# Optimization experiments

Hardware: AMD Instinct MI355X
Metric: run time of the kernel (lower is better)

## Reference

```python
import jax, jax.numpy as jnp
import numpy as np

B, IN, J, K = 1024, 512, 64, 8
CLAMP_MAX = 10.0

def setup_inputs() -> dict:
    key = jax.random.key(0)
    k1, k2 = jax.random.split(key)
    x = jax.random.normal(k1, (B, IN), dtype=jnp.float32)
    T = jax.random.normal(k2, (IN, J, K), dtype=jnp.float32)
    return {"x": x, "T": T}

def reference(x, T):
    # M: [B, J, K]
    M = jnp.einsum('bi,ijk->bjk', x, T)
    # pairwise diff over batch: [B, B, J, K] (matches torch broadcast M1-M2)
    diff = M[None, :, :, :] - M[:, None, :, :]
    sq = jnp.sum(diff * diff, axis=3)          # [B, B, J]
    # safe sqrt (grad 0 at 0, matching torch.norm subgradient on diagonal)
    sq_safe = jnp.where(sq > 0, sq, 1.0)
    norm = jnp.where(sq > 0, jnp.sqrt(sq_safe), 0.0)
    c = jnp.exp(-jnp.minimum(norm, CLAMP_MAX))  # clamp(max=10) then exp(-.)
    feats = jnp.sum(c, axis=1)                  # [B, J]
    return jnp.concatenate([x, feats], axis=1)  # [B, IN + J]
```

## Files before the change

kernel.cpp:

```cpp
#include <hip/hip_runtime.h>

constexpr int NB  = 1024;
constexpr int NIN = 512;
constexpr int NJ  = 64;
constexpr int NK  = 8;
constexpr int NC  = NJ * NK;
constexpr int OUTC = NIN + NJ;
constexpr float EXPN10 = 4.5399929762484854e-05f;
constexpr float FEAT_BASE = 1024.0f * EXPN10;

typedef __bf16 bf16x8 __attribute__((ext_vector_type(8)));
typedef float floatx16 __attribute__((ext_vector_type(16)));

__device__ __forceinline__ unsigned f2bf(float f) {
  unsigned u = __float_as_uint(f);
  u += 0x7FFFu + ((u >> 16) & 1u);
  return u >> 16;
}

__global__ __launch_bounds__(256) void conv_init_kernel(const float* __restrict__ x,
                                                        const float* __restrict__ T,
                                                        uint4* __restrict__ xb,
                                                        ushort* __restrict__ Tt,
                                                        float* __restrict__ out) {
  __shared__ float Ts[64][65];
  const int bid = blockIdx.x;
  const int tid = threadIdx.x;

  if (bid < 256) {
    const int idx = bid * 256 + tid;
    const float4 v0 = ((const float4*)x)[idx * 2];
    const float4 v1 = ((const float4*)x)[idx * 2 + 1];
    uint4 p;
    p.x = f2bf(v0.x) | (f2bf(v0.y) << 16);
    p.y = f2bf(v0.z) | (f2bf(v0.w) << 16);
    p.z = f2bf(v1.x) | (f2bf(v1.y) << 16);
    p.w = f2bf(v1.z) | (f2bf(v1.w) << 16);
    xb[idx] = p;
  } else if (bid < 320) {
    const int t = bid - 256;
    const int i0 = (t & 7) * 64;
    const int c0 = (t >> 3) * 64;

    const int ti4 = (tid >> 4) * 4;
    const int tc  = (tid & 15) * 4;
#pragma unroll
    for (int r = 0; r < 4; ++r) {
      const float4 v = *(const float4*)&T[(i0 + ti4 + r) * NC + c0 + tc];
      Ts[tc + 0][ti4 + r] = v.x;
      Ts[tc + 1][ti4 + r] = v.y;
      Ts[tc + 2][ti4 + r] = v.z;
      Ts[tc + 3][ti4 + r] = v.w;
    }
    __syncthreads();

    const int co = tid >> 2;
    const int io = (tid & 3) * 16;
    unsigned w[8];
#pragma unroll
    for (int q = 0; q < 8; ++q)
      w[q] = f2bf(Ts[co][io + 2 * q]) | (f2bf(Ts[co][io + 2 * q + 1]) << 16);
    uint4* dst = (uint4*)&Tt[(size_t)(c0 + co) * NIN + i0 + io];
    dst[0] = uint4{w[0], w[1], w[2], w[3]};
    dst[1] = uint4{w[4], w[5], w[6], w[7]};
  } else {
    const int idx = (bid - 320) * 256 + tid;
    const int b = idx / OUTC;
    const int c = idx - b * OUTC;
    out[idx] = (c < NIN) ? x[b * NIN + c] : FEAT_BASE;
  }
}

__global__ __launch_bounds__(256) void gemm_kernel(const uint4* __restrict__ xb,
                                                   const uint4* __restrict__ ttb,
                                                   float* __restrict__ Mp,
                                                   uint4* __restrict__ Mb,
                                                   float* __restrict__ na) {
  __shared__ __align__(16) ushort smem_u[2 * 64 * 136];
  ushort* Xs = smem_u;
  ushort* Ts = smem_u + 64 * 136;
  float*  Cs = (float*)smem_u;

  const int tid = threadIdx.x;
  const int b0 = blockIdx.x * 64;
  const int c0 = blockIdx.y * 64;

  const int lane = tid & 63;
  const int w    = tid >> 6;
  const int l31  = lane & 31;
  const int half = lane >> 5;
  const int arow = (w & 1) * 32 + l31;
  const int bcol = (w >> 1) * 32 + l31;

  floatx16 acc = {};

  for (int z = 0; z < 4; ++z) {
#pragma unroll
    for (int t = 0; t < 4; ++t) {
      const int u = t * 256 + tid;
      const int row = u >> 4, seg = u & 15;
      *(uint4*)&Xs[row * 136 + seg * 8] = xb[(b0 + row) * 64 + z * 16 + seg];
      *(uint4*)&Ts[row * 136 + seg * 8] = ttb[(c0 + row) * 64 + z * 16 + seg];
    }
    __syncthreads();

#pragma unroll
    for (int s = 0; s < 8; ++s) {
      const bf16x8 af = *(const bf16x8*)&Xs[arow * 136 + s * 16 + half * 8];
      const bf16x8 bf = *(const bf16x8*)&Ts[bcol * 136 + s * 16 + half * 8];
      acc = __builtin_amdgcn_mfma_f32_32x32x16_bf16(af, bf, acc, 0, 0, 0);
    }
    __syncthreads();
  }

#pragma unroll
  for (int reg = 0; reg < 16; ++reg) {
    const int row = (reg & 3) + 8 * (reg >> 2) + 4 * half;
    Cs[((w & 1) * 32 + row) * 68 + (w >> 1) * 32 + l31] = acc[reg];
  }
  __syncthreads();

#pragma unroll
  for (int pass = 0; pass < 2; ++pass) {
    const int jl = (tid >> 6) + pass * 4;
    const int b  = tid & 63;
    const float4 m0 = *(const float4*)&Cs[b * 68 + jl * 8];
    const float4 m1 = *(const float4*)&Cs[b * 68 + jl * 8 + 4];
    const int j_g = blockIdx.y * 8 + jl;
    const int idx = j_g * NB + b0 + b;
    ((float4*)Mp)[idx * 2]     = m0;
    ((float4*)Mp)[idx * 2 + 1] = m1;
    float s = m0.x * m0.x;
    s = fmaf(m0.y, m0.y, s); s = fmaf(m0.z, m0.z, s); s = fmaf(m0.w, m0.w, s);
    s = fmaf(m1.x, m1.x, s); s = fmaf(m1.y, m1.y, s); s = fmaf(m1.z, m1.z, s);
    s = fmaf(m1.w, m1.w, s);
    na[idx] = s;
    uint4 pk;
    pk.x = f2bf(m0.x) | (f2bf(m0.y) << 16);
    pk.y = f2bf(m0.z) | (f2bf(m0.w) << 16);
    pk.z = f2bf(m1.x) | (f2bf(m1.y) << 16);
    pk.w = f2bf(m1.z) | (f2bf(m1.w) << 16);
    Mb[idx] = pk;
  }
}

__global__ __launch_bounds__(256) void pairwise_kernel(const uint4* __restrict__ Mb,
                                                       const float* __restrict__ na,
                                                       const float* __restrict__ Mp,
                                                       float* __restrict__ out) {
  const int j    = blockIdx.x;
  const int ag   = blockIdx.y;
  const int bh   = blockIdx.z;
  const int tid  = threadIdx.x;
  const int lane = tid & 63;
  const int w    = tid >> 6;
  const int col  = lane & 31;
  const int h    = lane >> 5;
  const int jb   = j * NB;

  __shared__ uint4 Mb_s[513];
  __shared__ float nb_s[512];
  __shared__ float na_s[128];

  const int bbeg = bh * 512;
  Mb_s[tid]       = Mb[jb + bbeg + tid];
  Mb_s[tid + 256] = Mb[jb + bbeg + tid + 256];
  nb_s[tid]       = na[jb + bbeg + tid];
  nb_s[tid + 256] = na[jb + bbeg + tid + 256];
  if (tid == 0) Mb_s[512] = uint4{0u, 0u, 0u, 0u};

  const int a0 = ag * 128 + w * 32;
  if (lane < 32) na_s[w * 32 + lane] = na[jb + a0 + lane];

  uint4 araw = uint4{0u, 0u, 0u, 0u};
  if (lane < 32) araw = Mb[jb + a0 + lane];
  const bf16x8 af = __builtin_bit_cast(bf16x8, araw);

  __syncthreads();

  float c995[16];
#pragma unroll
  for (int reg = 0; reg < 16; ++reg) {
    const int row = (reg & 3) + 8 * (reg >> 2) + 4 * h;
    c995[reg] = 0.995f * na_s[w * 32 + row];
  }

  const floatx16 zero = {};

#pragma unroll 2
  for (int bt = 0; bt < 16; ++bt) {
    const int bidx = bt * 32 + col;
    const uint4 braw = Mb_s[lane < 32 ? bidx : 512];
    const bf16x8 bf = __builtin_bit_cast(bf16x8, braw);
    const floatx16 P = __builtin_amdgcn_mfma_f32_32x32x16_bf16(af, bf, zero, 0, 0, 0);
    const float nb_l = nb_s[bidx];
    const float rhs = 100.0f - 0.995f * nb_l;

    float t = fmaf(-2.0f, P[0], c995[0]);
#pragma unroll
    for (int reg = 1; reg < 16; ++reg)
      t = fminf(t, fmaf(-2.0f, P[reg], c995[reg]));

    if (__any(t < rhs)) {
#pragma unroll
      for (int reg = 0; reg < 16; ++reg) {
        if (fmaf(-2.0f, P[reg], c995[reg]) < rhs) {
          const int row = (reg & 3) + 8 * (reg >> 2) + 4 * h;
          const int a = a0 + row;
          const int b = bbeg + bt * 32 + col;
          float corr;
          if (a == b) {
            corr = 1.0f - EXPN10;
          } else {
            const float4 av0 = ((const float4*)Mp)[(jb + a) * 2];
            const float4 av1 = ((const float4*)Mp)[(jb + a) * 2 + 1];
            const float4 bv0 = ((const float4*)Mp)[(jb + b) * 2];
            const float4 bv1 = ((const float4*)Mp)[(jb + b) * 2 + 1];
            float d = av0.x - bv0.x; float sq = d * d;
            d = av0.y - bv0.y; sq = fmaf(d, d, sq);
            d = av0.z - bv0.z; sq = fmaf(d, d, sq);
            d = av0.w - bv0.w; sq = fmaf(d, d, sq);
            d = av1.x - bv1.x; sq = fmaf(d, d, sq);
            d = av1.y - bv1.y; sq = fmaf(d, d, sq);
            d = av1.z - bv1.z; sq = fmaf(d, d, sq);
            d = av1.w - bv1.w; sq = fmaf(d, d, sq);
            const float nrm = sqrtf(sq);
            corr = (nrm < 10.0f) ? (__expf(-nrm) - EXPN10) : 0.0f;
          }
          if (corr != 0.0f) atomicAdd(&out[a * OUTC + NIN + j], corr);
        }
      }
    }
  }
}

extern "C" void kernel_launch(void* const* d_in, const int* in_sizes, int n_in,
                              void* d_out, int out_size, void* d_ws, size_t ws_size,
                              hipStream_t stream) {
  const float* x = (const float*)d_in[0];
  const float* T = (const float*)d_in[1];
  float* out = (float*)d_out;

  float* Mp  = (float*)d_ws;
  float* na  = Mp + (size_t)NJ * NB * NK;
  uint4* Mb  = (uint4*)(na + (size_t)NJ * NB);
  uint4* xb  = Mb + (size_t)NJ * NB;
  ushort* Tt = (ushort*)(xb + (size_t)NB * NIN / 8);

  conv_init_kernel<<<dim3(2624), 256, 0, stream>>>(x, T, xb, Tt, out);
  gemm_kernel<<<dim3(16, 8), 256, 0, stream>>>(xb, (const uint4*)Tt, Mp, Mb, na);
  pairwise_kernel<<<dim3(NJ, 8, 2), 256, 0, stream>>>(Mb, na, Mp, out);
}
```

Baseline: 73.71 us.

## Fuse GEMM and pairwise kernels with a grid-wide atomic barrier

Merges the GEMM stage, the output initialisation (now float4-vectorised) and the pairwise stage into one persistent launch of 1024 blocks. A global atomic counter barrier, reset by the conversion kernel, separates the two phases. The aim is to remove one kernel launch and its inter-kernel gap and to overlap output init with the GEMM. It relies on all 1024 blocks being co-resident (launch bounds 256,4); otherwise the spin barrier can deadlock, and every block pays the barrier cost.

```diff
diff --git a/kernel.cpp b/kernel.cpp
--- a/kernel.cpp
+++ b/kernel.cpp
@@ -9,6 +9,8 @@
 constexpr float EXPN10 = 4.5399929762484854e-05f;
 constexpr float FEAT_BASE = 1024.0f * EXPN10;
 
+constexpr unsigned GRID2 = 1024;
+
 typedef __bf16 bf16x8 __attribute__((ext_vector_type(8)));
 typedef float floatx16 __attribute__((ext_vector_type(16)));
 
@@ -18,14 +20,16 @@
   return u >> 16;
 }
 
-__global__ __launch_bounds__(256) void conv_init_kernel(const float* __restrict__ x,
-                                                        const float* __restrict__ T,
-                                                        uint4* __restrict__ xb,
-                                                        ushort* __restrict__ Tt,
-                                                        float* __restrict__ out) {
+__global__ __launch_bounds__(256) void conv_kernel(const float* __restrict__ x,
+                                                   const float* __restrict__ T,
+                                                   uint4* __restrict__ xb,
+                                                   ushort* __restrict__ Tt,
+                                                   unsigned* __restrict__ cnt) {
   __shared__ float Ts[64][65];
   const int bid = blockIdx.x;
   const int tid = threadIdx.x;
+
+  if (bid == 0 && tid == 0) *cnt = 0u;
 
   if (bid < 256) {
     const int idx = bid * 256 + tid;
@@ -37,7 +41,7 @@
     p.z = f2bf(v1.x) | (f2bf(v1.y) << 16);
     p.w = f2bf(v1.z) | (f2bf(v1.w) << 16);
     xb[idx] = p;
-  } else if (bid < 320) {
+  } else {
     const int t = bid - 256;
     const int i0 = (t & 7) * 64;
     const int c0 = (t >> 3) * 64;
@@ -63,104 +67,120 @@
     uint4* dst = (uint4*)&Tt[(size_t)(c0 + co) * NIN + i0 + io];
     dst[0] = uint4{w[0], w[1], w[2], w[3]};
     dst[1] = uint4{w[4], w[5], w[6], w[7]};
+  }
+}
+
+__global__ __launch_bounds__(256, 4) void fused_kernel(const uint4* __restrict__ xb,
+                                                       const uint4* __restrict__ ttb,
+                                                       const float* __restrict__ x,
+                                                       float* __restrict__ Mp,
+                                                       uint4* __restrict__ Mb,
+                                                       float* __restrict__ na,
+                                                       float* __restrict__ out,
+                                                       unsigned* __restrict__ cnt) {
+  __shared__ __align__(16) unsigned char smem[2 * 64 * 136 * 2];
+  const int tid = threadIdx.x;
+  const int bid = blockIdx.x;
+
+  if (bid < 128) {
+    ushort* Xs = (ushort*)smem;
+    ushort* Ts = (ushort*)smem + 64 * 136;
+    float*  Cs = (float*)smem;
+
+    const int b0 = (bid & 15) * 64;
+    const int c0 = (bid >> 4) * 64;
+
+    const int lane = tid & 63;
+    const int w    = tid >> 6;
+    const int l31  = lane & 31;
+    const int half = lane >> 5;
+    const int arow = (w & 1) * 32 + l31;
+    const int bcol = (w >> 1) * 32 + l31;
+
+    floatx16 acc = {};
+
+    for (int z = 0; z < 4; ++z) {
+#pragma unroll
+      for (int t = 0; t < 4; ++t) {
+        const int u = t * 256 + tid;
+        const int row = u >> 4, seg = u & 15;
+        *(uint4*)&Xs[row * 136 + seg * 8] = xb[(b0 + row) * 64 + z * 16 + seg];
+        *(uint4*)&Ts[row * 136 + seg * 8] = ttb[(c0 + row) * 64 + z * 16 + seg];
+      }
+      __syncthreads();
+
+#pragma unroll
+      for (int s = 0; s < 8; ++s) {
+        const bf16x8 af = *(const bf16x8*)&Xs[arow * 136 + s * 16 + half * 8];
+        const bf16x8 bf = *(const bf16x8*)&Ts[bcol * 136 + s * 16 + half * 8];
+        acc = __builtin_amdgcn_mfma_f32_32x32x16_bf16(af, bf, acc, 0, 0, 0);
+      }
+      __syncthreads();
+    }
+
+#pragma unroll
+    for (int reg = 0; reg < 16; ++reg) {
+      const int row = (reg & 3) + 8 * (reg >> 2) + 4 * half;
+      Cs[((w & 1) * 32 + row) * 68 + (w >> 1) * 32 + l31] = acc[reg];
+    }
+    __syncthreads();
+
+#pragma unroll
+    for (int pass = 0; pass < 2; ++pass) {
+      const int jl = (tid >> 6) + pass * 4;
+      const int b  = tid & 63;
+      const float4 m0 = *(const float4*)&Cs[b * 68 + jl * 8];
+      const float4 m1 = *(const float4*)&Cs[b * 68 + jl * 8 + 4];
+      const int j_g = (bid >> 4) * 8 + jl;
+      const int idx = j_g * NB + b0 + b;
+      ((float4*)Mp)[idx * 2]     = m0;
+      ((float4*)Mp)[idx * 2 + 1] = m1;
+      float s = m0.x * m0.x;
+      s = fmaf(m0.y, m0.y, s); s = fmaf(m0.z, m0.z, s); s = fmaf(m0.w, m0.w, s);
+      s = fmaf(m1.x, m1.x, s); s = fmaf(m1.y, m1.y, s); s = fmaf(m1.z, m1.z, s);
+      s = fmaf(m1.w, m1.w, s);
+      na[idx] = s;
+      uint4 pk;
+      pk.x = f2bf(m0.x) | (f2bf(m0.y) << 16);
+      pk.y = f2bf(m0.z) | (f2bf(m0.w) << 16);
+      pk.z = f2bf(m1.x) | (f2bf(m1.y) << 16);
+      pk.w = f2bf(m1.z) | (f2bf(m1.w) << 16);
+      Mb[idx] = pk;
+    }
   } else {
-    const int idx = (bid - 320) * 256 + tid;
-    const int b = idx / OUTC;
-    const int c = idx - b * OUTC;
-    out[idx] = (c < NIN) ? x[b * NIN + c] : FEAT_BASE;
-  }
-}
-
-__global__ __launch_bounds__(256) void gemm_kernel(const uint4* __restrict__ xb,
-                                                   const uint4* __restrict__ ttb,
-                                                   float* __restrict__ Mp,
-                                                   uint4* __restrict__ Mb,
-                                                   float* __restrict__ na) {
-  __shared__ __align__(16) ushort smem_u[2 * 64 * 136];
-  ushort* Xs = smem_u;
-  ushort* Ts = smem_u + 64 * 136;
-  float*  Cs = (float*)smem_u;
-
-  const int tid = threadIdx.x;
-  const int b0 = blockIdx.x * 64;
-  const int c0 = blockIdx.y * 64;
-
-  const int lane = tid & 63;
-  const int w    = tid >> 6;
-  const int l31  = lane & 31;
-  const int half = lane >> 5;
-  const int arow = (w & 1) * 32 + l31;
-  const int bcol = (w >> 1) * 32 + l31;
-
-  floatx16 acc = {};
-
-  for (int z = 0; z < 4; ++z) {
-#pragma unroll
-    for (int t = 0; t < 4; ++t) {
-      const int u = t * 256 + tid;
-      const int row = u >> 4, seg = u & 15;
-      *(uint4*)&Xs[row * 136 + seg * 8] = xb[(b0 + row) * 64 + z * 16 + seg];
-      *(uint4*)&Ts[row * 136 + seg * 8] = ttb[(c0 + row) * 64 + z * 16 + seg];
-    }
-    __syncthreads();
-
-#pragma unroll
-    for (int s = 0; s < 8; ++s) {
-      const bf16x8 af = *(const bf16x8*)&Xs[arow * 136 + s * 16 + half * 8];
-      const bf16x8 bf = *(const bf16x8*)&Ts[bcol * 136 + s * 16 + half * 8];
-      acc = __builtin_amdgcn_mfma_f32_32x32x16_bf16(af, bf, acc, 0, 0, 0);
-    }
-    __syncthreads();
-  }
-
-#pragma unroll
-  for (int reg = 0; reg < 16; ++reg) {
-    const int row = (reg & 3) + 8 * (reg >> 2) + 4 * half;
-    Cs[((w & 1) * 32 + row) * 68 + (w >> 1) * 32 + l31] = acc[reg];
-  }
+    const int gi = (bid - 128) * 256 + tid;
+    if (gi < (NB * OUTC) / 4) {
+      const int b = gi / (OUTC / 4);
+      const int r = gi - b * (OUTC / 4);
+      float4 v;
+      if (r < NIN / 4) v = ((const float4*)x)[b * (NIN / 4) + r];
+      else v = float4{FEAT_BASE, FEAT_BASE, FEAT_BASE, FEAT_BASE};
+      ((float4*)out)[gi] = v;
+    }
+  }
+
   __syncthreads();
-
-#pragma unroll
-  for (int pass = 0; pass < 2; ++pass) {
-    const int jl = (tid >> 6) + pass * 4;
-    const int b  = tid & 63;
-    const float4 m0 = *(const float4*)&Cs[b * 68 + jl * 8];
-    const float4 m1 = *(const float4*)&Cs[b * 68 + jl * 8 + 4];
-    const int j_g = blockIdx.y * 8 + jl;
-    const int idx = j_g * NB + b0 + b;
-    ((float4*)Mp)[idx * 2]     = m0;
-    ((float4*)Mp)[idx * 2 + 1] = m1;
-    float s = m0.x * m0.x;
-    s = fmaf(m0.y, m0.y, s); s = fmaf(m0.z, m0.z, s); s = fmaf(m0.w, m0.w, s);
-    s = fmaf(m1.x, m1.x, s); s = fmaf(m1.y, m1.y, s); s = fmaf(m1.z, m1.z, s);
-    s = fmaf(m1.w, m1.w, s);
-    na[idx] = s;
-    uint4 pk;
-    pk.x = f2bf(m0.x) | (f2bf(m0.y) << 16);
-    pk.y = f2bf(m0.z) | (f2bf(m0.w) << 16);
-    pk.z = f2bf(m1.x) | (f2bf(m1.y) << 16);
-    pk.w = f2bf(m1.z) | (f2bf(m1.w) << 16);
-    Mb[idx] = pk;
-  }
-}
-
-__global__ __launch_bounds__(256) void pairwise_kernel(const uint4* __restrict__ Mb,
-                                                       const float* __restrict__ na,
-                                                       const float* __restrict__ Mp,
-                                                       float* __restrict__ out) {
-  const int j    = blockIdx.x;
-  const int ag   = blockIdx.y;
-  const int bh   = blockIdx.z;
-  const int tid  = threadIdx.x;
+  if (tid == 0) {
+    __threadfence();
+    __hip_atomic_fetch_add(cnt, 1u, __ATOMIC_ACQ_REL, __HIP_MEMORY_SCOPE_AGENT);
+    while (__hip_atomic_load(cnt, __ATOMIC_ACQUIRE, __HIP_MEMORY_SCOPE_AGENT) < GRID2)
+      __builtin_amdgcn_s_sleep(2);
+    __threadfence();
+  }
+  __syncthreads();
+
+  const int j    = bid & 63;
+  const int ag   = (bid >> 6) & 7;
+  const int bh   = bid >> 9;
   const int lane = tid & 63;
   const int w    = tid >> 6;
   const int col  = lane & 31;
   const int h    = lane >> 5;
   const int jb   = j * NB;
 
-  __shared__ uint4 Mb_s[513];
-  __shared__ float nb_s[512];
-  __shared__ float na_s[128];
+  uint4* Mb_s = (uint4*)smem;
+  float* nb_s = (float*)(smem + 8208);
+  float* na_s = (float*)(smem + 10256);
 
   const int bbeg = bh * 512;
   Mb_s[tid]       = Mb[jb + bbeg + tid];
@@ -246,8 +266,8 @@
   uint4* Mb  = (uint4*)(na + (size_t)NJ * NB);
   uint4* xb  = Mb + (size_t)NJ * NB;
   ushort* Tt = (ushort*)(xb + (size_t)NB * NIN / 8);
-
-  conv_init_kernel<<<dim3(2624), 256, 0, stream>>>(x, T, xb, Tt, out);
-  gemm_kernel<<<dim3(16, 8), 256, 0, stream>>>(xb, (const uint4*)Tt, Mp, Mb, na);
-  pairwise_kernel<<<dim3(NJ, 8, 2), 256, 0, stream>>>(Mb, na, Mp, out);
-}
+  unsigned* cnt = (unsigned*)((char*)d_ws + (8u << 20));
+
+  conv_kernel<<<dim3(320), 256, 0, stream>>>(x, T, xb, Tt, cnt);
+  fused_kernel<<<dim3(GRID2), 256, 0, stream>>>(xb, (const uint4*)Tt, x, Mp, Mb, na, out, cnt);
+}
```

Result: slower. 205.8 us (+179.2%).

## Fuse bf16 conversion and output init into the GEMM kernel

Applied to the files above, without the earlier changes.

Removes the separate conversion/init kernel and has the GEMM read fp32 x and T directly, converting them to bf16 while staging into shared memory. Each GEMM block also writes its share of the output initialisation (x copy plus base feature value). This saves one kernel launch and the round trip of the bf16 intermediates through global memory. In exchange, x and T are re-read and re-converted redundantly across blocks, and the T staging uses scalar strided loads with 2-byte shared stores.

```diff
diff --git a/kernel.cpp b/kernel.cpp
--- a/kernel.cpp
+++ b/kernel.cpp
@@ -18,64 +18,12 @@
   return u >> 16;
 }
 
-__global__ __launch_bounds__(256) void conv_init_kernel(const float* __restrict__ x,
-                                                        const float* __restrict__ T,
-                                                        uint4* __restrict__ xb,
-                                                        ushort* __restrict__ Tt,
-                                                        float* __restrict__ out) {
-  __shared__ float Ts[64][65];
-  const int bid = blockIdx.x;
-  const int tid = threadIdx.x;
-
-  if (bid < 256) {
-    const int idx = bid * 256 + tid;
-    const float4 v0 = ((const float4*)x)[idx * 2];
-    const float4 v1 = ((const float4*)x)[idx * 2 + 1];
-    uint4 p;
-    p.x = f2bf(v0.x) | (f2bf(v0.y) << 16);
-    p.y = f2bf(v0.z) | (f2bf(v0.w) << 16);
-    p.z = f2bf(v1.x) | (f2bf(v1.y) << 16);
-    p.w = f2bf(v1.z) | (f2bf(v1.w) << 16);
-    xb[idx] = p;
-  } else if (bid < 320) {
-    const int t = bid - 256;
-    const int i0 = (t & 7) * 64;
-    const int c0 = (t >> 3) * 64;
-
-    const int ti4 = (tid >> 4) * 4;
-    const int tc  = (tid & 15) * 4;
-#pragma unroll
-    for (int r = 0; r < 4; ++r) {
-      const float4 v = *(const float4*)&T[(i0 + ti4 + r) * NC + c0 + tc];
-      Ts[tc + 0][ti4 + r] = v.x;
-      Ts[tc + 1][ti4 + r] = v.y;
-      Ts[tc + 2][ti4 + r] = v.z;
-      Ts[tc + 3][ti4 + r] = v.w;
-    }
-    __syncthreads();
-
-    const int co = tid >> 2;
-    const int io = (tid & 3) * 16;
-    unsigned w[8];
-#pragma unroll
-    for (int q = 0; q < 8; ++q)
-      w[q] = f2bf(Ts[co][io + 2 * q]) | (f2bf(Ts[co][io + 2 * q + 1]) << 16);
-    uint4* dst = (uint4*)&Tt[(size_t)(c0 + co) * NIN + i0 + io];
-    dst[0] = uint4{w[0], w[1], w[2], w[3]};
-    dst[1] = uint4{w[4], w[5], w[6], w[7]};
-  } else {
-    const int idx = (bid - 320) * 256 + tid;
-    const int b = idx / OUTC;
-    const int c = idx - b * OUTC;
-    out[idx] = (c < NIN) ? x[b * NIN + c] : FEAT_BASE;
-  }
-}
-
-__global__ __launch_bounds__(256) void gemm_kernel(const uint4* __restrict__ xb,
-                                                   const uint4* __restrict__ ttb,
-                                                   float* __restrict__ Mp,
-                                                   uint4* __restrict__ Mb,
-                                                   float* __restrict__ na) {
+__global__ __launch_bounds__(256) void gemm_fused(const float* __restrict__ x,
+                                                  const float* __restrict__ T,
+                                                  float* __restrict__ Mp,
+                                                  uint4* __restrict__ Mb,
+                                                  float* __restrict__ na,
+                                                  float* __restrict__ out) {
   __shared__ __align__(16) ushort smem_u[2 * 64 * 136];
   ushort* Xs = smem_u;
   ushort* Ts = smem_u + 64 * 136;
@@ -92,16 +40,46 @@
   const int arow = (w & 1) * 32 + l31;
   const int bcol = (w >> 1) * 32 + l31;
 
+  const int bidf = blockIdx.y * 16 + blockIdx.x;
+#pragma unroll
+  for (int it = 0; it < 5; ++it) {
+    const int li = it * 256 + tid;
+    if (li < 1152) {
+      const int gi = bidf * 1152 + li;
+      const int b = gi / (OUTC / 4);
+      const int r = gi - b * (OUTC / 4);
+      float4 v;
+      if (r < NIN / 4) v = ((const float4*)x)[b * (NIN / 4) + r];
+      else v = float4{FEAT_BASE, FEAT_BASE, FEAT_BASE, FEAT_BASE};
+      ((float4*)out)[gi] = v;
+    }
+  }
+
   floatx16 acc = {};
 
   for (int z = 0; z < 4; ++z) {
 #pragma unroll
     for (int t = 0; t < 4; ++t) {
       const int u = t * 256 + tid;
-      const int row = u >> 4, seg = u & 15;
-      *(uint4*)&Xs[row * 136 + seg * 8] = xb[(b0 + row) * 64 + z * 16 + seg];
-      *(uint4*)&Ts[row * 136 + seg * 8] = ttb[(c0 + row) * 64 + z * 16 + seg];
-    }
+      const int row = u >> 4;
+      const int seg = u & 15;
+      const float4 v0 = *(const float4*)&x[(size_t)(b0 + row) * NIN + z * 128 + seg * 8];
+      const float4 v1 = *(const float4*)&x[(size_t)(b0 + row) * NIN + z * 128 + seg * 8 + 4];
+      uint4 p;
+      p.x = f2bf(v0.x) | (f2bf(v0.y) << 16);
+      p.y = f2bf(v0.z) | (f2bf(v0.w) << 16);
+      p.z = f2bf(v1.x) | (f2bf(v1.y) << 16);
+      p.w = f2bf(v1.z) | (f2bf(v1.w) << 16);
+      *(uint4*)&Xs[row * 136 + seg * 8] = p;
+    }
+
+#pragma unroll
+    for (int i = 0; i < 32; ++i) {
+      const int kk = i * 4 + w;
+      const float v = T[(size_t)(z * 128 + kk) * NC + c0 + lane];
+      Ts[lane * 136 + kk] = (ushort)f2bf(v);
+    }
+
     __syncthreads();
 
 #pragma unroll
@@ -244,10 +222,7 @@
   float* Mp  = (float*)d_ws;
   float* na  = Mp + (size_t)NJ * NB * NK;
   uint4* Mb  = (uint4*)(na + (size_t)NJ * NB);
-  uint4* xb  = Mb + (size_t)NJ * NB;
-  ushort* Tt = (ushort*)(xb + (size_t)NB * NIN / 8);
-
-  conv_init_kernel<<<dim3(2624), 256, 0, stream>>>(x, T, xb, Tt, out);
-  gemm_kernel<<<dim3(16, 8), 256, 0, stream>>>(xb, (const uint4*)Tt, Mp, Mb, na);
+
+  gemm_fused<<<dim3(16, 8), 256, 0, stream>>>(x, T, Mp, Mb, na, out);
   pairwise_kernel<<<dim3(NJ, 8, 2), 256, 0, stream>>>(Mb, na, Mp, out);
 }
```

Result: slower. 106.3 us (+44.2%).
